# Kernel tuning notes

Hardware: AMD Instinct MI355X
Metric: run time of the kernel (lower is better)

## Reference

```python
import jax, jax.numpy as jnp
import numpy as np

EPS = 1e-5
H = 8
N_BUCKETS = 32


def _instance_norm(x, gamma, beta):
    # x: [B, N, D]; torch InstanceNorm1d normalizes over the N (length) dim
    # per channel per batch element, using biased variance.
    m = jnp.mean(x, axis=1, keepdims=True)
    v = jnp.var(x, axis=1, keepdims=True)
    return (x - m) * jax.lax.rsqrt(v + EPS) * gamma + beta


def setup_inputs() -> dict:
    key = jax.random.key(0)
    ks = jax.random.split(key, 12)
    B, N, D, d_ff = 4, 512, 128, 512
    s = 1.0 / np.sqrt(D)
    sf = 1.0 / np.sqrt(d_ff)
    u = lambda k, shape, lim: jax.random.uniform(k, shape, jnp.float32, -lim, lim)
    return {
        "h": jax.random.normal(ks[0], (B, N, D), jnp.float32),
        "coords": jax.random.uniform(ks[1], (B, N, 2), jnp.float32),
        "W_Q": u(ks[2], (D, D), s),
        "W_K": u(ks[3], (D, D), s),
        "W_V": u(ks[4], (D, D), s),
        "W_O": u(ks[5], (D, D), s),
        "emb": jax.random.normal(ks[6], (N_BUCKETS, D), jnp.float32),  # n_heads*d_k == D
        "ffn_w1": u(ks[7], (D, d_ff), s),
        "ffn_b1": u(ks[8], (d_ff,), s),
        "ffn_w2": u(ks[9], (d_ff, D), sf),
        "ffn_b2": u(ks[10], (D,), sf),
        "gamma1": jnp.ones((D,), jnp.float32),
        "beta1": jnp.zeros((D,), jnp.float32),
        "gamma2": jnp.ones((D,), jnp.float32),
        "beta2": jnp.zeros((D,), jnp.float32),
    }


def reference(h, coords, W_Q, W_K, W_V, W_O, emb, ffn_w1, ffn_b1, ffn_w2,
              ffn_b2, gamma1, beta1, gamma2, beta2):
    B, N, D = h.shape
    Dk = D // H
    Q = (h @ W_Q).reshape(B, N, H, Dk)
    K = (h @ W_K).reshape(B, N, H, Dk)
    V = (h @ W_V).reshape(B, N, H, Dk)
    # content scores: [B, H, N, N]
    scores = jnp.einsum('bnhd,bmhd->bhnm', Q, K) / np.sqrt(Dk)
    # relative-distance bucket embeddings for all (i, j) pairs
    diff = coords[:, :, None, :] - coords[:, None, :, :]          # [B,N,N,2]
    dist = jax.lax.stop_gradient(jnp.sqrt(jnp.sum(diff * diff, -1)))
    buckets = jnp.clip((dist * N_BUCKETS).astype(jnp.int32), 0, N_BUCKETS - 1)
    r = emb[buckets].reshape(B, N, N, H, Dk)                      # [B,N,N,H,Dk]
    scores = scores + jnp.einsum('bnhd,bnmhd->bhnm', Q, r)
    attn = jax.nn.softmax(scores, axis=-1)
    h_attn = jnp.einsum('bhnm,bmhd->bnhd', attn, V).reshape(B, N, D) @ W_O
    h1 = _instance_norm(h + h_attn, gamma1, beta1)
    h_ffn = jax.nn.relu(h1 @ ffn_w1 + ffn_b1) @ ffn_w2 + ffn_b2
    return _instance_norm(h1 + h_ffn, gamma2, beta2)
```

## Files before the change

### kernel.cpp

```cpp
#include <hip/hip_runtime.h>
#include <hip/hip_bf16.h>

#define B_  4
#define N_  512
#define D_  128
#define H_  8
#define DK  16
#define DFF 512
#define NB  32
#define KS  8
#define FS  8

__global__ __launch_bounds__(256) void qkv_qe_kernel(
    const float* __restrict__ A,
    const float* __restrict__ WQ, const float* __restrict__ WK, const float* __restrict__ WV,
    const float* __restrict__ emb,
    float* __restrict__ Qo, float* __restrict__ Ko, float* __restrict__ Vo,
    float* __restrict__ QE)
{
    const float* Bw = blockIdx.z == 0 ? WQ : (blockIdx.z == 1 ? WK : WV);
    float*       C  = blockIdx.z == 0 ? Qo : (blockIdx.z == 1 ? Ko : Vo);
    const int wave = threadIdx.x >> 6;
    const int lane = threadIdx.x & 63;
    const int rbase = __builtin_amdgcn_readfirstlane((blockIdx.x * 4 + wave) * 2);
    const int col = lane * 2;

    float acc[2][2] = {};
#pragma unroll 2
    for (int k0 = 0; k0 < D_; k0 += 4) {
        float4 a0 = *(const float4*)&A[(size_t)(rbase + 0) * D_ + k0];
        float4 a1 = *(const float4*)&A[(size_t)(rbase + 1) * D_ + k0];
#pragma unroll
        for (int kk = 0; kk < 4; ++kk) {
            float2 bv = *(const float2*)&Bw[(size_t)(k0 + kk) * D_ + col];
            float x0 = (&a0.x)[kk], x1 = (&a1.x)[kk];
            acc[0][0] += x0 * bv.x; acc[0][1] += x0 * bv.y;
            acc[1][0] += x1 * bv.x; acc[1][1] += x1 * bv.y;
        }
    }
    *(float2*)&C[(size_t)(rbase + 0) * D_ + col] = make_float2(acc[0][0], acc[0][1]);
    *(float2*)&C[(size_t)(rbase + 1) * D_ + col] = make_float2(acc[1][0], acc[1][1]);

    if (blockIdx.z == 0) {
        __shared__ float Qls[8][132];
        *(float2*)&Qls[wave * 2 + 0][col] = make_float2(acc[0][0], acc[0][1]);
        *(float2*)&Qls[wave * 2 + 1][col] = make_float2(acc[1][0], acc[1][1]);
        __syncthreads();
        const int r  = threadIdx.x >> 5;
        const int hh = (threadIdx.x >> 2) & 7;
        const int k0 = (threadIdx.x & 3) * 8;
        const int grow = blockIdx.x * 8 + r;
        const float4* qv = (const float4*)&Qls[r][hh * DK];
        const float4 qa = qv[0], qb = qv[1], qc = qv[2], qd = qv[3];
        float* qe_out = QE + ((size_t)grow * H_ + hh) * NB + k0;
#pragma unroll 2
        for (int k = 0; k < 8; ++k) {
            const float4* ep = (const float4*)(emb + (size_t)(k0 + k) * D_ + hh * DK);
            float4 e0 = ep[0], e1 = ep[1], e2 = ep[2], e3 = ep[3];
            float dot = qa.x*e0.x + qa.y*e0.y + qa.z*e0.z + qa.w*e0.w
                      + qb.x*e1.x + qb.y*e1.y + qb.z*e1.z + qb.w*e1.w
                      + qc.x*e2.x + qc.y*e2.y + qc.z*e2.z + qc.w*e2.w
                      + qd.x*e3.x + qd.y*e3.y + qd.z*e3.z + qd.w*e3.w;
            qe_out[k] = dot;
        }
    }
}

__global__ __launch_bounds__(256) void attn6_kernel(
    const float* __restrict__ Q, const float* __restrict__ K, const float* __restrict__ V,
    const float* __restrict__ QE, const float* __restrict__ coords,
    float* __restrict__ P)
{
    const int tid  = threadIdx.x;
    const int wave = tid >> 6;
    const int lane = tid & 63;
    const int bid  = blockIdx.x;
    const int ks    = bid & 7;
    const int chunk = (bid >> 3) & 7;
    const int h     = (bid >> 6) & (H_ - 1);
    const int b     = bid >> 9;

    const int n   = chunk * 64 + lane;
    const int row = b * N_ + n;

    __shared__ float kl[64][16];
    __shared__ float vl[64][16];
    __shared__ float qel[64][NB + 1];
    __shared__ float ckrd[64][2];
    __shared__ float accl[4][64][17];

    const size_t hdbase = (size_t)b * N_ * D_ + h * DK;

    {
        int key = tid >> 2, part = tid & 3;
        size_t g = hdbase + (size_t)(ks * 64 + key) * D_ + part * 4;
        *(float4*)&kl[key][part * 4] = *(const float4*)&K[g];
        *(float4*)&vl[key][part * 4] = *(const float4*)&V[g];
    }
    {
        int r = tid >> 2, part = tid & 3;
        const float* src = QE + ((size_t)(b * N_ + chunk * 64 + r) * H_ + h) * NB + part * 8;
#pragma unroll
        for (int j = 0; j < 8; ++j) qel[r][part * 8 + j] = src[j];
    }
    if (tid < 128)
        ((float*)ckrd)[tid] = coords[(size_t)(b * N_ + ks * 64) * 2 + tid];

    const float4* qp = (const float4*)(Q + (size_t)row * D_ + h * DK);
    const float4 q0 = qp[0], q1 = qp[1], q2 = qp[2], q3 = qp[3];
    const float cx = coords[(size_t)row * 2 + 0];
    const float cy = coords[(size_t)row * 2 + 1];

    __syncthreads();

    float l = 0.f;
    float acc[16] = {};

    const int ml0 = wave * 16;
#pragma unroll 4
    for (int i = 0; i < 16; ++i) {
        const int ml = ml0 + i;
        const float4* kp = (const float4*)&kl[ml][0];
        const float4 k0 = kp[0], k1 = kp[1], k2 = kp[2], k3 = kp[3];
        float dot = q0.x*k0.x + q0.y*k0.y + q0.z*k0.z + q0.w*k0.w
                  + q1.x*k1.x + q1.y*k1.y + q1.z*k1.z + q1.w*k1.w
                  + q2.x*k2.x + q2.y*k2.y + q2.z*k2.z + q2.w*k2.w
                  + q3.x*k3.x + q3.y*k3.y + q3.z*k3.z + q3.w*k3.w;
        float dx = cx - ckrd[ml][0], dy = cy - ckrd[ml][1];
        float dist = sqrtf(dx * dx + dy * dy);
        int bucket = (int)(dist * 32.0f);
        bucket = bucket > (NB - 1) ? (NB - 1) : bucket;
        float s = dot * 0.25f + qel[lane][bucket];
        float p = __expf(s);
        l += p;
        const float4* vp = (const float4*)&vl[ml][0];
        const float4 v0 = vp[0], v1 = vp[1], v2 = vp[2], v3 = vp[3];
        acc[0]  += p * v0.x; acc[1]  += p * v0.y; acc[2]  += p * v0.z; acc[3]  += p * v0.w;
        acc[4]  += p * v1.x; acc[5]  += p * v1.y; acc[6]  += p * v1.z; acc[7]  += p * v1.w;
        acc[8]  += p * v2.x; acc[9]  += p * v2.y; acc[10] += p * v2.z; acc[11] += p * v2.w;
        acc[12] += p * v3.x; acc[13] += p * v3.y; acc[14] += p * v3.z; acc[15] += p * v3.w;
    }

    accl[wave][lane][16] = l;
#pragma unroll
    for (int j = 0; j < 16; ++j) accl[wave][lane][j] = acc[j];
    __syncthreads();

    float* pb = P + (size_t)bid * (64 * 17);
    for (int i = tid; i < 64 * 17; i += 256) {
        int r = i / 17, j = i - r * 17;
        pb[i] = accl[0][r][j] + accl[1][r][j] + accl[2][r][j] + accl[3][r][j];
    }
}

__global__ __launch_bounds__(256) void oproj_kernel(
    const float* __restrict__ P, const float* __restrict__ WO,
    const float* __restrict__ hres, float* __restrict__ X1)
{
    const int tid = threadIdx.x;
    const int gr0 = blockIdx.x * 8;
    __shared__ float AOls[8][128];
    __shared__ float lsl[8][8];

    if (tid < 64) {
        int r = tid >> 3, hh = tid & 7;
        int gr = gr0 + r;
        int b = gr >> 9, n = gr & (N_ - 1);
        int chunk = n >> 6, rl = n & 63;
        size_t base = ((size_t)(((b * H_ + hh) * 8 + chunk) * KS)) * (64 * 17) + (size_t)rl * 17;
        float l = 0.f;
#pragma unroll
        for (int s = 0; s < KS; ++s) l += P[base + (size_t)s * (64 * 17) + 16];
        lsl[r][hh] = l;
    }

    float asum[4];
#pragma unroll
    for (int j = 0; j < 4; ++j) {
        int i = tid + j * 256;
        int r = i >> 7, d = i & 127;
        int gr = gr0 + r;
        int b = gr >> 9, n = gr & (N_ - 1);
        int chunk = n >> 6, rl = n & 63;
        int hh = d >> 4, dk = d & 15;
        size_t base = ((size_t)(((b * H_ + hh) * 8 + chunk) * KS)) * (64 * 17) + (size_t)rl * 17 + dk;
        float a = 0.f;
#pragma unroll
        for (int s = 0; s < KS; ++s) a += P[base + (size_t)s * (64 * 17)];
        asum[j] = a;
    }
    __syncthreads();
#pragma unroll
    for (int j = 0; j < 4; ++j) {
        int i = tid + j * 256;
        int r = i >> 7, d = i & 127;
        AOls[r][d] = asum[j] / lsl[r][d >> 4];
    }
    __syncthreads();

    const int wave = tid >> 6;
    const int lane = tid & 63;
    const int rl = wave * 2;
    const int grb = __builtin_amdgcn_readfirstlane(gr0 + rl);
    const int col = lane * 2;

    float acc[2][2] = {};
#pragma unroll 2
    for (int k0 = 0; k0 < D_; k0 += 4) {
        float4 a0 = *(const float4*)&AOls[rl + 0][k0];
        float4 a1 = *(const float4*)&AOls[rl + 1][k0];
#pragma unroll
        for (int kk = 0; kk < 4; ++kk) {
            float2 bv = *(const float2*)&WO[(size_t)(k0 + kk) * D_ + col];
            float x0 = (&a0.x)[kk], x1 = (&a1.x)[kk];
            acc[0][0] += x0 * bv.x; acc[0][1] += x0 * bv.y;
            acc[1][0] += x1 * bv.x; acc[1][1] += x1 * bv.y;
        }
    }
#pragma unroll
    for (int j = 0; j < 2; ++j) {
        float2 rv = *(const float2*)&hres[(size_t)(grb + j) * D_ + col];
        *(float2*)&X1[(size_t)(grb + j) * D_ + col] =
            make_float2(acc[j][0] + rv.x, acc[j][1] + rv.y);
    }
}

__global__ __launch_bounds__(256) void stats_kernel(const float* __restrict__ X,
    const float* __restrict__ gamma, const float* __restrict__ beta,
    float* __restrict__ T1, float* __restrict__ T2)
{
    const int b  = blockIdx.x >> 5;
    const int dg = blockIdx.x & 31;
    const int dl = threadIdx.x & 3;
    const int nc = threadIdx.x >> 2;
    const float* xp = X + ((size_t)b * N_ + nc * 8) * D_ + dg * 4 + dl;
    float s = 0.f, q = 0.f;
#pragma unroll
    for (int i = 0; i < 8; ++i) { float x = xp[(size_t)i * D_]; s += x; q += x * x; }
    __shared__ float rs[64][4], rq[64][4];
    rs[nc][dl] = s; rq[nc][dl] = q;
    __syncthreads();
    for (int off = 32; off >= 1; off >>= 1) {
        if (nc < off) { rs[nc][dl] += rs[nc + off][dl]; rq[nc][dl] += rq[nc + off][dl]; }
        __syncthreads();
    }
    if (threadIdx.x < 4) {
        int d = dg * 4 + threadIdx.x;
        float mean = rs[0][threadIdx.x] * (1.0f / N_);
        float var  = rq[0][threadIdx.x] * (1.0f / N_) - mean * mean;
        float r = 1.0f / sqrtf(var + 1e-5f);
        float t1 = r * gamma[d];
        T1[b * D_ + d] = t1;
        T2[b * D_ + d] = beta[d] - mean * t1;
    }
}

__global__ __launch_bounds__(256) void ffn1_kernel(
    const float* __restrict__ X1, const float* __restrict__ T1, const float* __restrict__ T2,
    const float* __restrict__ w1, const float* __restrict__ b1, float* __restrict__ F1)
{
    __shared__ float Als[16][128];
    const int gr0 = blockIdx.x * 16;
    const int b = gr0 >> 9;
#pragma unroll
    for (int i = threadIdx.x * 4; i < 16 * 128; i += 1024) {
        int r = i >> 7, c = i & 127;
        float4 x  = *(const float4*)&X1[(size_t)(gr0 + r) * D_ + c];
        float4 t1 = *(const float4*)&T1[b * D_ + c];
        float4 t2 = *(const float4*)&T2[b * D_ + c];
        float4 y;
        y.x = x.x * t1.x + t2.x; y.y = x.y * t1.y + t2.y;
        y.z = x.z * t1.z + t2.z; y.w = x.w * t1.w + t2.w;
        *(float4*)&Als[r][c] = y;
    }
    __syncthreads();

    const int wave = threadIdx.x >> 6;
    const int lane = threadIdx.x & 63;
    const int rl = wave * 4;
    const int grb = __builtin_amdgcn_readfirstlane(gr0 + rl);
    const int col = blockIdx.y * 128 + lane * 2;

    float acc[4][2] = {};
#pragma unroll 2
    for (int k0 = 0; k0 < D_; k0 += 4) {
        float4 a4[4];
#pragma unroll
        for (int j = 0; j < 4; ++j) a4[j] = *(const float4*)&Als[rl + j][k0];
#pragma unroll
        for (int kk = 0; kk < 4; ++kk) {
            float2 bv = *(const float2*)&w1[(size_t)(k0 + kk) * DFF + col];
#pragma unroll
            for (int j = 0; j < 4; ++j) {
                float a = (&a4[j].x)[kk];
                acc[j][0] += a * bv.x;
                acc[j][1] += a * bv.y;
            }
        }
    }
    float2 bb = *(const float2*)&b1[col];
#pragma unroll
    for (int j = 0; j < 4; ++j) {
        float o0 = fmaxf(acc[j][0] + bb.x, 0.f);
        float o1 = fmaxf(acc[j][1] + bb.y, 0.f);
        *(float2*)&F1[(size_t)(grb + j) * DFF + col] = make_float2(o0, o1);
    }
}

__global__ __launch_bounds__(256) void ffn2s_kernel(
    const float* __restrict__ F1, const float* __restrict__ w2, float* __restrict__ Pf)
{
    const int wave = threadIdx.x >> 6;
    const int lane = threadIdx.x & 63;
    const int rbase = __builtin_amdgcn_readfirstlane((blockIdx.x * 4 + wave) * 4);
    const int col = lane * 2;
    const int s = blockIdx.z;
    const int kbeg = s * (DFF / FS);

    float acc[4][2] = {};
#pragma unroll 2
    for (int k0 = kbeg; k0 < kbeg + DFF / FS; k0 += 4) {
        float4 a4[4];
#pragma unroll
        for (int j = 0; j < 4; ++j)
            a4[j] = *(const float4*)&F1[(size_t)(rbase + j) * DFF + k0];
#pragma unroll
        for (int kk = 0; kk < 4; ++kk) {
            float2 bv = *(const float2*)&w2[(size_t)(k0 + kk) * D_ + col];
#pragma unroll
            for (int j = 0; j < 4; ++j) {
                float a = (&a4[j].x)[kk];
                acc[j][0] += a * bv.x;
                acc[j][1] += a * bv.y;
            }
        }
    }
#pragma unroll
    for (int j = 0; j < 4; ++j)
        *(float2*)&Pf[((size_t)s * (B_ * N_) + rbase + j) * D_ + col] =
            make_float2(acc[j][0], acc[j][1]);
}

__global__ __launch_bounds__(256) void fcomb_kernel(
    const float* __restrict__ Pf, const float* __restrict__ b2,
    const float* __restrict__ X1, const float* __restrict__ T1, const float* __restrict__ T2,
    float* __restrict__ X2)
{
    int idx = (blockIdx.x * 256 + threadIdx.x) * 4;
    int d = idx & (D_ - 1);
    int b = idx >> 16;
    float4 o  = *(const float4*)&b2[d];
    float4 x1 = *(const float4*)&X1[idx];
    float4 t1 = *(const float4*)&T1[b * D_ + d];
    float4 t2 = *(const float4*)&T2[b * D_ + d];
    o.x += x1.x * t1.x + t2.x; o.y += x1.y * t1.y + t2.y;
    o.z += x1.z * t1.z + t2.z; o.w += x1.w * t1.w + t2.w;
#pragma unroll
    for (int s = 0; s < FS; ++s) {
        float4 p = *(const float4*)&Pf[(size_t)s * (B_ * N_ * D_) + idx];
        o.x += p.x; o.y += p.y; o.z += p.z; o.w += p.w;
    }
    *(float4*)&X2[idx] = o;
}

__global__ __launch_bounds__(256) void stats_apply_kernel(const float* __restrict__ X,
    const float* __restrict__ gamma, const float* __restrict__ beta,
    float* __restrict__ Y)
{
    const int b  = blockIdx.x >> 5;
    const int dg = blockIdx.x & 31;
    const int dl = threadIdx.x & 3;
    const int nc = threadIdx.x >> 2;
    const float* xp = X + ((size_t)b * N_ + nc * 8) * D_ + dg * 4 + dl;
    float s = 0.f, q = 0.f;
#pragma unroll
    for (int i = 0; i < 8; ++i) { float x = xp[(size_t)i * D_]; s += x; q += x * x; }
    __shared__ float rs[64][4], rq[64][4];
    __shared__ float t1l[4], t2l[4];
    rs[nc][dl] = s; rq[nc][dl] = q;
    __syncthreads();
    for (int off = 32; off >= 1; off >>= 1) {
        if (nc < off) { rs[nc][dl] += rs[nc + off][dl]; rq[nc][dl] += rq[nc + off][dl]; }
        __syncthreads();
    }
    if (threadIdx.x < 4) {
        int d = dg * 4 + threadIdx.x;
        float mean = rs[0][threadIdx.x] * (1.0f / N_);
        float var  = rq[0][threadIdx.x] * (1.0f / N_) - mean * mean;
        float r = 1.0f / sqrtf(var + 1e-5f);
        float t1 = r * gamma[d];
        t1l[threadIdx.x] = t1;
        t2l[threadIdx.x] = beta[d] - mean * t1;
    }
    __syncthreads();
    const float t1 = t1l[dl], t2 = t2l[dl];
    float* yp = Y + ((size_t)b * N_ + nc * 8) * D_ + dg * 4 + dl;
#pragma unroll
    for (int i = 0; i < 8; ++i) yp[(size_t)i * D_] = xp[(size_t)i * D_] * t1 + t2;
}

extern "C" void kernel_launch(void* const* d_in, const int* in_sizes, int n_in,
                              void* d_out, int out_size, void* d_ws, size_t ws_size,
                              hipStream_t stream)
{
    const float* h      = (const float*)d_in[0];
    const float* coords = (const float*)d_in[1];
    const float* W_Q    = (const float*)d_in[2];
    const float* W_K    = (const float*)d_in[3];
    const float* W_V    = (const float*)d_in[4];
    const float* W_O    = (const float*)d_in[5];
    const float* emb    = (const float*)d_in[6];
    const float* w1     = (const float*)d_in[7];
    const float* b1     = (const float*)d_in[8];
    const float* w2     = (const float*)d_in[9];
    const float* b2     = (const float*)d_in[10];
    const float* g1     = (const float*)d_in[11];
    const float* be1    = (const float*)d_in[12];
    const float* g2     = (const float*)d_in[13];
    const float* be2    = (const float*)d_in[14];
    float* out = (float*)d_out;

    float* ws = (float*)d_ws;
    const size_t R = (size_t)B_ * N_;
    float* Qb  = ws;
    float* Kb  = Qb + R * D_;
    float* Vb  = Kb + R * D_;
    float* QEb = Vb + R * D_;
    float* X1  = QEb + R * H_ * NB;
    float* F1  = X1 + R * D_;
    float* X2  = F1 + R * DFF;
    float* Pb  = X2 + R * D_;
    float* Pf  = Pb + (size_t)2048 * 64 * 17;
    float* T1a = Pf + (size_t)FS * R * D_;
    float* T2a = T1a + B_ * D_;

    qkv_qe_kernel<<<dim3(256, 1, 3), 256, 0, stream>>>(
        h, W_Q, W_K, W_V, emb, Qb, Kb, Vb, QEb);
    attn6_kernel<<<dim3(2048), 256, 0, stream>>>(Qb, Kb, Vb, QEb, coords, Pb);
    oproj_kernel<<<dim3((int)R / 8), 256, 0, stream>>>(Pb, W_O, h, X1);
    stats_kernel<<<dim3(B_ * 32), 256, 0, stream>>>(X1, g1, be1, T1a, T2a);
    ffn1_kernel<<<dim3(128, 4), 256, 0, stream>>>(X1, T1a, T2a, w1, b1, F1);
    ffn2s_kernel<<<dim3(128, 1, FS), 256, 0, stream>>>(F1, w2, Pf);
    fcomb_kernel<<<dim3((int)(R * D_) / 1024), 256, 0, stream>>>(Pf, b2, X1, T1a, T2a, X2);
    stats_apply_kernel<<<dim3(B_ * 32), 256, 0, stream>>>(X2, g2, be2, out);
}
```

Before: 84.56 us.

## Halve attention key splits, loop two key tiles per block, retile oproj

Result: no change. 86.20 us (+1.9%).

```diff
diff --git a/kernel.cpp b/kernel.cpp
--- a/kernel.cpp
+++ b/kernel.cpp
@@ -8,8 +8,8 @@
 #define DK  16
 #define DFF 512
 #define NB  32
-#define KS  8
-#define FS  8
+#define KS  4
+#define FS  4
 
 __global__ __launch_bounds__(256) void qkv_qe_kernel(
     const float* __restrict__ A,
@@ -57,16 +57,16 @@
         for (int k = 0; k < 8; ++k) {
             const float4* ep = (const float4*)(emb + (size_t)(k0 + k) * D_ + hh * DK);
             float4 e0 = ep[0], e1 = ep[1], e2 = ep[2], e3 = ep[3];
-            float dot = qa.x*e0.x + qa.y*e0.y + qa.z*e0.z + qa.w*e0.w
-                      + qb.x*e1.x + qb.y*e1.y + qb.z*e1.z + qb.w*e1.w
-                      + qc.x*e2.x + qc.y*e2.y + qc.z*e2.z + qc.w*e2.w
-                      + qd.x*e3.x + qd.y*e3.y + qd.z*e3.z + qd.w*e3.w;
-            qe_out[k] = dot;
-        }
-    }
-}
-
-__global__ __launch_bounds__(256) void attn6_kernel(
+            float d0 = fmaf(qa.x,e0.x, fmaf(qa.y,e0.y, fmaf(qa.z,e0.z, qa.w*e0.w)));
+            float d1 = fmaf(qb.x,e1.x, fmaf(qb.y,e1.y, fmaf(qb.z,e1.z, qb.w*e1.w)));
+            float d2 = fmaf(qc.x,e2.x, fmaf(qc.y,e2.y, fmaf(qc.z,e2.z, qc.w*e2.w)));
+            float d3 = fmaf(qd.x,e3.x, fmaf(qd.y,e3.y, fmaf(qd.z,e3.z, qd.w*e3.w)));
+            qe_out[k] = (d0 + d1) + (d2 + d3);
+        }
+    }
+}
+
+__global__ __launch_bounds__(256) void attn7_kernel(
     const float* __restrict__ Q, const float* __restrict__ K, const float* __restrict__ V,
     const float* __restrict__ QE, const float* __restrict__ coords,
     float* __restrict__ P)
@@ -75,72 +75,74 @@
     const int wave = tid >> 6;
     const int lane = tid & 63;
     const int bid  = blockIdx.x;
-    const int ks    = bid & 7;
-    const int chunk = (bid >> 3) & 7;
-    const int h     = (bid >> 6) & (H_ - 1);
-    const int b     = bid >> 9;
-
-    const int n   = chunk * 64 + lane;
-    const int row = b * N_ + n;
+    const int ks    = bid & 3;
+    const int chunk = (bid >> 2) & 7;
+    const int h     = (bid >> 5) & (H_ - 1);
+    const int b     = bid >> 8;
+    const int row = b * N_ + chunk * 64 + lane;
 
     __shared__ float kl[64][16];
     __shared__ float vl[64][16];
     __shared__ float qel[64][NB + 1];
-    __shared__ float ckrd[64][2];
+    __shared__ float ckrd[128][2];
     __shared__ float accl[4][64][17];
 
     const size_t hdbase = (size_t)b * N_ * D_ + h * DK;
 
-    {
-        int key = tid >> 2, part = tid & 3;
-        size_t g = hdbase + (size_t)(ks * 64 + key) * D_ + part * 4;
-        *(float4*)&kl[key][part * 4] = *(const float4*)&K[g];
-        *(float4*)&vl[key][part * 4] = *(const float4*)&V[g];
-    }
     {
         int r = tid >> 2, part = tid & 3;
         const float* src = QE + ((size_t)(b * N_ + chunk * 64 + r) * H_ + h) * NB + part * 8;
 #pragma unroll
         for (int j = 0; j < 8; ++j) qel[r][part * 8 + j] = src[j];
     }
-    if (tid < 128)
-        ((float*)ckrd)[tid] = coords[(size_t)(b * N_ + ks * 64) * 2 + tid];
+    ((float*)ckrd)[tid] = coords[(size_t)(b * N_ + ks * 128) * 2 + tid];
 
     const float4* qp = (const float4*)(Q + (size_t)row * D_ + h * DK);
     const float4 q0 = qp[0], q1 = qp[1], q2 = qp[2], q3 = qp[3];
     const float cx = coords[(size_t)row * 2 + 0];
     const float cy = coords[(size_t)row * 2 + 1];
 
-    __syncthreads();
-
     float l = 0.f;
     float acc[16] = {};
 
-    const int ml0 = wave * 16;
+    for (int rnd = 0; rnd < 2; ++rnd) {
+        if (rnd) __syncthreads();
+        {
+            int key = tid >> 2, part = tid & 3;
+            size_t g = hdbase + (size_t)(ks * 128 + rnd * 64 + key) * D_ + part * 4;
+            *(float4*)&kl[key][part * 4] = *(const float4*)&K[g];
+            *(float4*)&vl[key][part * 4] = *(const float4*)&V[g];
+        }
+        __syncthreads();
+
+        const int ml0 = wave * 16;
 #pragma unroll 4
-    for (int i = 0; i < 16; ++i) {
-        const int ml = ml0 + i;
-        const float4* kp = (const float4*)&kl[ml][0];
-        const float4 k0 = kp[0], k1 = kp[1], k2 = kp[2], k3 = kp[3];
-        float dot = q0.x*k0.x + q0.y*k0.y + q0.z*k0.z + q0.w*k0.w
-                  + q1.x*k1.x + q1.y*k1.y + q1.z*k1.z + q1.w*k1.w
-                  + q2.x*k2.x + q2.y*k2.y + q2.z*k2.z + q2.w*k2.w
-                  + q3.x*k3.x + q3.y*k3.y + q3.z*k3.z + q3.w*k3.w;
-        float dx = cx - ckrd[ml][0], dy = cy - ckrd[ml][1];
-        float dist = sqrtf(dx * dx + dy * dy);
-        int bucket = (int)(dist * 32.0f);
-        bucket = bucket > (NB - 1) ? (NB - 1) : bucket;
-        float s = dot * 0.25f + qel[lane][bucket];
-        float p = __expf(s);
-        l += p;
-        const float4* vp = (const float4*)&vl[ml][0];
-        const float4 v0 = vp[0], v1 = vp[1], v2 = vp[2], v3 = vp[3];
-        acc[0]  += p * v0.x; acc[1]  += p * v0.y; acc[2]  += p * v0.z; acc[3]  += p * v0.w;
-        acc[4]  += p * v1.x; acc[5]  += p * v1.y; acc[6]  += p * v1.z; acc[7]  += p * v1.w;
-        acc[8]  += p * v2.x; acc[9]  += p * v2.y; acc[10] += p * v2.z; acc[11] += p * v2.w;
-        acc[12] += p * v3.x; acc[13] += p * v3.y; acc[14] += p * v3.z; acc[15] += p * v3.w;
-    }
-
+        for (int i = 0; i < 16; ++i) {
+            const int ml = ml0 + i;
+            const int mc = rnd * 64 + ml;
+            float dx = cx - ckrd[mc][0], dy = cy - ckrd[mc][1];
+            float dist = sqrtf(fmaf(dx, dx, dy * dy));
+            int bucket = (int)(dist * 32.0f);
+            bucket = bucket > (NB - 1) ? (NB - 1) : bucket;
+            float qe = qel[lane][bucket];
+            const float4* kp = (const float4*)&kl[ml][0];
+            const float4 k0 = kp[0], k1 = kp[1], k2 = kp[2], k3 = kp[3];
+            float d0 = fmaf(q0.x,k0.x, fmaf(q0.y,k0.y, fmaf(q0.z,k0.z, q0.w*k0.w)));
+            float d1 = fmaf(q1.x,k1.x, fmaf(q1.y,k1.y, fmaf(q1.z,k1.z, q1.w*k1.w)));
+            float d2 = fmaf(q2.x,k2.x, fmaf(q2.y,k2.y, fmaf(q2.z,k2.z, q2.w*k2.w)));
+            float d3 = fmaf(q3.x,k3.x, fmaf(q3.y,k3.y, fmaf(q3.z,k3.z, q3.w*k3.w)));
+            float p = __expf(fmaf((d0 + d1) + (d2 + d3), 0.25f, qe));
+            l += p;
+            const float4* vp = (const float4*)&vl[ml][0];
+            const float4 v0 = vp[0], v1 = vp[1], v2 = vp[2], v3 = vp[3];
+            acc[0]  += p * v0.x; acc[1]  += p * v0.y; acc[2]  += p * v0.z; acc[3]  += p * v0.w;
+            acc[4]  += p * v1.x; acc[5]  += p * v1.y; acc[6]  += p * v1.z; acc[7]  += p * v1.w;
+            acc[8]  += p * v2.x; acc[9]  += p * v2.y; acc[10] += p * v2.z; acc[11] += p * v2.w;
+            acc[12] += p * v3.x; acc[13] += p * v3.y; acc[14] += p * v3.z; acc[15] += p * v3.w;
+        }
+    }
+
+    __syncthreads();
     accl[wave][lane][16] = l;
 #pragma unroll
     for (int j = 0; j < 16; ++j) accl[wave][lane][j] = acc[j];
@@ -158,11 +160,11 @@
     const float* __restrict__ hres, float* __restrict__ X1)
 {
     const int tid = threadIdx.x;
-    const int gr0 = blockIdx.x * 8;
-    __shared__ float AOls[8][128];
-    __shared__ float lsl[8][8];
-
-    if (tid < 64) {
+    const int gr0 = blockIdx.x * 4;
+    __shared__ float AOls[4][128];
+    __shared__ float lsl[4][8];
+
+    if (tid < 32) {
         int r = tid >> 3, hh = tid & 7;
         int gr = gr0 + r;
         int b = gr >> 9, n = gr & (N_ - 1);
@@ -173,10 +175,9 @@
         for (int s = 0; s < KS; ++s) l += P[base + (size_t)s * (64 * 17) + 16];
         lsl[r][hh] = l;
     }
-
-    float asum[4];
-#pragma unroll
-    for (int j = 0; j < 4; ++j) {
+    float asum[2];
+#pragma unroll
+    for (int j = 0; j < 2; ++j) {
         int i = tid + j * 256;
         int r = i >> 7, d = i & 127;
         int gr = gr0 + r;
@@ -184,14 +185,14 @@
         int chunk = n >> 6, rl = n & 63;
         int hh = d >> 4, dk = d & 15;
         size_t base = ((size_t)(((b * H_ + hh) * 8 + chunk) * KS)) * (64 * 17) + (size_t)rl * 17 + dk;
-        float a = 0.f;
-#pragma unroll
-        for (int s = 0; s < KS; ++s) a += P[base + (size_t)s * (64 * 17)];
-        asum[j] = a;
-    }
-    __syncthreads();
-#pragma unroll
-    for (int j = 0; j < 4; ++j) {
+        float s = 0.f;
+#pragma unroll
+        for (int ss = 0; ss < KS; ++ss) s += P[base + (size_t)ss * (64 * 17)];
+        asum[j] = s;
+    }
+    __syncthreads();
+#pragma unroll
+    for (int j = 0; j < 2; ++j) {
         int i = tid + j * 256;
         int r = i >> 7, d = i & 127;
         AOls[r][d] = asum[j] / lsl[r][d >> 4];
@@ -200,29 +201,21 @@
 
     const int wave = tid >> 6;
     const int lane = tid & 63;
-    const int rl = wave * 2;
-    const int grb = __builtin_amdgcn_readfirstlane(gr0 + rl);
     const int col = lane * 2;
-
-    float acc[2][2] = {};
+    float acc0 = 0.f, acc1 = 0.f;
 #pragma unroll 2
     for (int k0 = 0; k0 < D_; k0 += 4) {
-        float4 a0 = *(const float4*)&AOls[rl + 0][k0];
-        float4 a1 = *(const float4*)&AOls[rl + 1][k0];
+        float4 av = *(const float4*)&AOls[wave][k0];
 #pragma unroll
         for (int kk = 0; kk < 4; ++kk) {
             float2 bv = *(const float2*)&WO[(size_t)(k0 + kk) * D_ + col];
-            float x0 = (&a0.x)[kk], x1 = (&a1.x)[kk];
-            acc[0][0] += x0 * bv.x; acc[0][1] += x0 * bv.y;
-            acc[1][0] += x1 * bv.x; acc[1][1] += x1 * bv.y;
-        }
-    }
-#pragma unroll
-    for (int j = 0; j < 2; ++j) {
-        float2 rv = *(const float2*)&hres[(size_t)(grb + j) * D_ + col];
-        *(float2*)&X1[(size_t)(grb + j) * D_ + col] =
-            make_float2(acc[j][0] + rv.x, acc[j][1] + rv.y);
-    }
+            float x = (&av.x)[kk];
+            acc0 += x * bv.x; acc1 += x * bv.y;
+        }
+    }
+    const int gr = gr0 + wave;
+    float2 rv = *(const float2*)&hres[(size_t)gr * D_ + col];
+    *(float2*)&X1[(size_t)gr * D_ + col] = make_float2(acc0 + rv.x, acc1 + rv.y);
 }
 
 __global__ __launch_bounds__(256) void stats_kernel(const float* __restrict__ X,
@@ -278,7 +271,6 @@
     const int wave = threadIdx.x >> 6;
     const int lane = threadIdx.x & 63;
     const int rl = wave * 4;
-    const int grb = __builtin_amdgcn_readfirstlane(gr0 + rl);
     const int col = blockIdx.y * 128 + lane * 2;
 
     float acc[4][2] = {};
@@ -292,9 +284,8 @@
             float2 bv = *(const float2*)&w1[(size_t)(k0 + kk) * DFF + col];
 #pragma unroll
             for (int j = 0; j < 4; ++j) {
-                float a = (&a4[j].x)[kk];
-                acc[j][0] += a * bv.x;
-                acc[j][1] += a * bv.y;
+                float x = (&a4[j].x)[kk];
+                acc[j][0] += x * bv.x; acc[j][1] += x * bv.y;
             }
         }
     }
@@ -303,7 +294,7 @@
     for (int j = 0; j < 4; ++j) {
         float o0 = fmaxf(acc[j][0] + bb.x, 0.f);
         float o1 = fmaxf(acc[j][1] + bb.y, 0.f);
-        *(float2*)&F1[(size_t)(grb + j) * DFF + col] = make_float2(o0, o1);
+        *(float2*)&F1[(size_t)(gr0 + rl + j) * DFF + col] = make_float2(o0, o1);
     }
 }
 
@@ -329,9 +320,8 @@
             float2 bv = *(const float2*)&w2[(size_t)(k0 + kk) * D_ + col];
 #pragma unroll
             for (int j = 0; j < 4; ++j) {
-                float a = (&a4[j].x)[kk];
-                acc[j][0] += a * bv.x;
-                acc[j][1] += a * bv.y;
+                float x = (&a4[j].x)[kk];
+                acc[j][0] += x * bv.x; acc[j][1] += x * bv.y;
             }
         }
     }
@@ -430,14 +420,14 @@
     float* F1  = X1 + R * D_;
     float* X2  = F1 + R * DFF;
     float* Pb  = X2 + R * D_;
-    float* Pf  = Pb + (size_t)2048 * 64 * 17;
+    float* Pf  = Pb + (size_t)1024 * 64 * 17;
     float* T1a = Pf + (size_t)FS * R * D_;
     float* T2a = T1a + B_ * D_;
 
     qkv_qe_kernel<<<dim3(256, 1, 3), 256, 0, stream>>>(
         h, W_Q, W_K, W_V, emb, Qb, Kb, Vb, QEb);
-    attn6_kernel<<<dim3(2048), 256, 0, stream>>>(Qb, Kb, Vb, QEb, coords, Pb);
-    oproj_kernel<<<dim3((int)R / 8), 256, 0, stream>>>(Pb, W_O, h, X1);
+    attn7_kernel<<<dim3(1024), 256, 0, stream>>>(Qb, Kb, Vb, QEb, coords, Pb);
+    oproj_kernel<<<dim3((int)R / 4), 256, 0, stream>>>(Pb, W_O, h, X1);
     stats_kernel<<<dim3(B_ * 32), 256, 0, stream>>>(X1, g1, be1, T1a, T2a);
     ffn1_kernel<<<dim3(128, 4), 256, 0, stream>>>(X1, T1a, T2a, w1, b1, F1);
     ffn2s_kernel<<<dim3(128, 1, FS), 256, 0, stream>>>(F1, w2, Pf);
```

## Fuse FFN2 split-K reduction and residual combine into one kernel via LDS

Applied to the files above, without the earlier changes.

New measurement: 80.73 us. 1.05x faster.

```diff
diff --git a/kernel.cpp b/kernel.cpp
--- a/kernel.cpp
+++ b/kernel.cpp
@@ -9,7 +9,6 @@
 #define DFF 512
 #define NB  32
 #define KS  8
-#define FS  8
 
 __global__ __launch_bounds__(256) void qkv_qe_kernel(
     const float* __restrict__ A,
@@ -57,11 +56,11 @@
         for (int k = 0; k < 8; ++k) {
             const float4* ep = (const float4*)(emb + (size_t)(k0 + k) * D_ + hh * DK);
             float4 e0 = ep[0], e1 = ep[1], e2 = ep[2], e3 = ep[3];
-            float dot = qa.x*e0.x + qa.y*e0.y + qa.z*e0.z + qa.w*e0.w
-                      + qb.x*e1.x + qb.y*e1.y + qb.z*e1.z + qb.w*e1.w
-                      + qc.x*e2.x + qc.y*e2.y + qc.z*e2.z + qc.w*e2.w
-                      + qd.x*e3.x + qd.y*e3.y + qd.z*e3.z + qd.w*e3.w;
-            qe_out[k] = dot;
+            float d0 = fmaf(qa.x,e0.x, fmaf(qa.y,e0.y, fmaf(qa.z,e0.z, qa.w*e0.w)));
+            float d1 = fmaf(qb.x,e1.x, fmaf(qb.y,e1.y, fmaf(qb.z,e1.z, qb.w*e1.w)));
+            float d2 = fmaf(qc.x,e2.x, fmaf(qc.y,e2.y, fmaf(qc.z,e2.z, qc.w*e2.w)));
+            float d3 = fmaf(qd.x,e3.x, fmaf(qd.y,e3.y, fmaf(qd.z,e3.z, qd.w*e3.w)));
+            qe_out[k] = (d0 + d1) + (d2 + d3);
         }
     }
 }
@@ -79,9 +78,7 @@
     const int chunk = (bid >> 3) & 7;
     const int h     = (bid >> 6) & (H_ - 1);
     const int b     = bid >> 9;
-
-    const int n   = chunk * 64 + lane;
-    const int row = b * N_ + n;
+    const int row = b * N_ + chunk * 64 + lane;
 
     __shared__ float kl[64][16];
     __shared__ float vl[64][16];
@@ -90,7 +87,6 @@
     __shared__ float accl[4][64][17];
 
     const size_t hdbase = (size_t)b * N_ * D_ + h * DK;
-
     {
         int key = tid >> 2, part = tid & 3;
         size_t g = hdbase + (size_t)(ks * 64 + key) * D_ + part * 4;
@@ -115,23 +111,22 @@
 
     float l = 0.f;
     float acc[16] = {};
-
     const int ml0 = wave * 16;
 #pragma unroll 4
     for (int i = 0; i < 16; ++i) {
         const int ml = ml0 + i;
+        float dx = cx - ckrd[ml][0], dy = cy - ckrd[ml][1];
+        float dist = sqrtf(fmaf(dx, dx, dy * dy));
+        int bucket = (int)(dist * 32.0f);
+        bucket = bucket > (NB - 1) ? (NB - 1) : bucket;
+        float qe = qel[lane][bucket];
         const float4* kp = (const float4*)&kl[ml][0];
         const float4 k0 = kp[0], k1 = kp[1], k2 = kp[2], k3 = kp[3];
-        float dot = q0.x*k0.x + q0.y*k0.y + q0.z*k0.z + q0.w*k0.w
-                  + q1.x*k1.x + q1.y*k1.y + q1.z*k1.z + q1.w*k1.w
-                  + q2.x*k2.x + q2.y*k2.y + q2.z*k2.z + q2.w*k2.w
-                  + q3.x*k3.x + q3.y*k3.y + q3.z*k3.z + q3.w*k3.w;
-        float dx = cx - ckrd[ml][0], dy = cy - ckrd[ml][1];
-        float dist = sqrtf(dx * dx + dy * dy);
-        int bucket = (int)(dist * 32.0f);
-        bucket = bucket > (NB - 1) ? (NB - 1) : bucket;
-        float s = dot * 0.25f + qel[lane][bucket];
-        float p = __expf(s);
+        float d0 = fmaf(q0.x,k0.x, fmaf(q0.y,k0.y, fmaf(q0.z,k0.z, q0.w*k0.w)));
+        float d1 = fmaf(q1.x,k1.x, fmaf(q1.y,k1.y, fmaf(q1.z,k1.z, q1.w*k1.w)));
+        float d2 = fmaf(q2.x,k2.x, fmaf(q2.y,k2.y, fmaf(q2.z,k2.z, q2.w*k2.w)));
+        float d3 = fmaf(q3.x,k3.x, fmaf(q3.y,k3.y, fmaf(q3.z,k3.z, q3.w*k3.w)));
+        float p = __expf(fmaf((d0 + d1) + (d2 + d3), 0.25f, qe));
         l += p;
         const float4* vp = (const float4*)&vl[ml][0];
         const float4 v0 = vp[0], v1 = vp[1], v2 = vp[2], v3 = vp[3];
@@ -173,7 +168,6 @@
         for (int s = 0; s < KS; ++s) l += P[base + (size_t)s * (64 * 17) + 16];
         lsl[r][hh] = l;
     }
-
     float asum[4];
 #pragma unroll
     for (int j = 0; j < 4; ++j) {
@@ -184,10 +178,10 @@
         int chunk = n >> 6, rl = n & 63;
         int hh = d >> 4, dk = d & 15;
         size_t base = ((size_t)(((b * H_ + hh) * 8 + chunk) * KS)) * (64 * 17) + (size_t)rl * 17 + dk;
-        float a = 0.f;
-#pragma unroll
-        for (int s = 0; s < KS; ++s) a += P[base + (size_t)s * (64 * 17)];
-        asum[j] = a;
+        float s = 0.f;
+#pragma unroll
+        for (int ss = 0; ss < KS; ++ss) s += P[base + (size_t)ss * (64 * 17)];
+        asum[j] = s;
     }
     __syncthreads();
 #pragma unroll
@@ -278,7 +272,6 @@
     const int wave = threadIdx.x >> 6;
     const int lane = threadIdx.x & 63;
     const int rl = wave * 4;
-    const int grb = __builtin_amdgcn_readfirstlane(gr0 + rl);
     const int col = blockIdx.y * 128 + lane * 2;
 
     float acc[4][2] = {};
@@ -292,9 +285,8 @@
             float2 bv = *(const float2*)&w1[(size_t)(k0 + kk) * DFF + col];
 #pragma unroll
             for (int j = 0; j < 4; ++j) {
-                float a = (&a4[j].x)[kk];
-                acc[j][0] += a * bv.x;
-                acc[j][1] += a * bv.y;
+                float x = (&a4[j].x)[kk];
+                acc[j][0] += x * bv.x; acc[j][1] += x * bv.y;
             }
         }
     }
@@ -303,64 +295,57 @@
     for (int j = 0; j < 4; ++j) {
         float o0 = fmaxf(acc[j][0] + bb.x, 0.f);
         float o1 = fmaxf(acc[j][1] + bb.y, 0.f);
-        *(float2*)&F1[(size_t)(grb + j) * DFF + col] = make_float2(o0, o1);
-    }
-}
-
-__global__ __launch_bounds__(256) void ffn2s_kernel(
-    const float* __restrict__ F1, const float* __restrict__ w2, float* __restrict__ Pf)
-{
-    const int wave = threadIdx.x >> 6;
-    const int lane = threadIdx.x & 63;
-    const int rbase = __builtin_amdgcn_readfirstlane((blockIdx.x * 4 + wave) * 4);
+        *(float2*)&F1[(size_t)(gr0 + rl + j) * DFF + col] = make_float2(o0, o1);
+    }
+}
+
+__global__ __launch_bounds__(256) void ffn2f_kernel(
+    const float* __restrict__ F1, const float* __restrict__ w2, const float* __restrict__ b2,
+    const float* __restrict__ X1, const float* __restrict__ T1, const float* __restrict__ T2,
+    float* __restrict__ X2)
+{
+    const int tid = threadIdx.x;
+    const int wave = tid >> 6;
+    const int lane = tid & 63;
+    const int gr0 = __builtin_amdgcn_readfirstlane(blockIdx.x * 4);
+    const int kbeg = __builtin_amdgcn_readfirstlane(wave * 128);
     const int col = lane * 2;
-    const int s = blockIdx.z;
-    const int kbeg = s * (DFF / FS);
+
+    __shared__ float part[4][4][128];
 
     float acc[4][2] = {};
 #pragma unroll 2
-    for (int k0 = kbeg; k0 < kbeg + DFF / FS; k0 += 4) {
+    for (int k0 = kbeg; k0 < kbeg + 128; k0 += 4) {
         float4 a4[4];
 #pragma unroll
         for (int j = 0; j < 4; ++j)
-            a4[j] = *(const float4*)&F1[(size_t)(rbase + j) * DFF + k0];
+            a4[j] = *(const float4*)&F1[(size_t)(gr0 + j) * DFF + k0];
 #pragma unroll
         for (int kk = 0; kk < 4; ++kk) {
             float2 bv = *(const float2*)&w2[(size_t)(k0 + kk) * D_ + col];
 #pragma unroll
             for (int j = 0; j < 4; ++j) {
-                float a = (&a4[j].x)[kk];
-                acc[j][0] += a * bv.x;
-                acc[j][1] += a * bv.y;
+                float x = (&a4[j].x)[kk];
+                acc[j][0] += x * bv.x; acc[j][1] += x * bv.y;
             }
         }
     }
 #pragma unroll
     for (int j = 0; j < 4; ++j)
-        *(float2*)&Pf[((size_t)s * (B_ * N_) + rbase + j) * D_ + col] =
-            make_float2(acc[j][0], acc[j][1]);
-}
-
-__global__ __launch_bounds__(256) void fcomb_kernel(
-    const float* __restrict__ Pf, const float* __restrict__ b2,
-    const float* __restrict__ X1, const float* __restrict__ T1, const float* __restrict__ T2,
-    float* __restrict__ X2)
-{
-    int idx = (blockIdx.x * 256 + threadIdx.x) * 4;
-    int d = idx & (D_ - 1);
-    int b = idx >> 16;
-    float4 o  = *(const float4*)&b2[d];
-    float4 x1 = *(const float4*)&X1[idx];
-    float4 t1 = *(const float4*)&T1[b * D_ + d];
-    float4 t2 = *(const float4*)&T2[b * D_ + d];
-    o.x += x1.x * t1.x + t2.x; o.y += x1.y * t1.y + t2.y;
-    o.z += x1.z * t1.z + t2.z; o.w += x1.w * t1.w + t2.w;
-#pragma unroll
-    for (int s = 0; s < FS; ++s) {
-        float4 p = *(const float4*)&Pf[(size_t)s * (B_ * N_ * D_) + idx];
-        o.x += p.x; o.y += p.y; o.z += p.z; o.w += p.w;
-    }
-    *(float4*)&X2[idx] = o;
+        *(float2*)&part[wave][j][col] = make_float2(acc[j][0], acc[j][1]);
+    __syncthreads();
+
+#pragma unroll
+    for (int e = 0; e < 2; ++e) {
+        int i = tid + e * 256;
+        int r = i >> 7, c = i & 127;
+        int row = gr0 + r;
+        int b = row >> 9;
+        float s = part[0][r][c] + part[1][r][c] + part[2][r][c] + part[3][r][c];
+        float x1 = X1[(size_t)row * D_ + c];
+        float o = s + b2[c] + (x1 * T1[b * D_ + c] + T2[b * D_ + c]);
+        X2[(size_t)row * D_ + c] = o;
+    }
 }
 
 __global__ __launch_bounds__(256) void stats_apply_kernel(const float* __restrict__ X,
@@ -430,8 +415,7 @@
     float* F1  = X1 + R * D_;
     float* X2  = F1 + R * DFF;
     float* Pb  = X2 + R * D_;
-    float* Pf  = Pb + (size_t)2048 * 64 * 17;
-    float* T1a = Pf + (size_t)FS * R * D_;
+    float* T1a = Pb + (size_t)2048 * 64 * 17;
     float* T2a = T1a + B_ * D_;
 
     qkv_qe_kernel<<<dim3(256, 1, 3), 256, 0, stream>>>(
@@ -440,7 +424,6 @@
     oproj_kernel<<<dim3((int)R / 8), 256, 0, stream>>>(Pb, W_O, h, X1);
     stats_kernel<<<dim3(B_ * 32), 256, 0, stream>>>(X1, g1, be1, T1a, T2a);
     ffn1_kernel<<<dim3(128, 4), 256, 0, stream>>>(X1, T1a, T2a, w1, b1, F1);
-    ffn2s_kernel<<<dim3(128, 1, FS), 256, 0, stream>>>(F1, w2, Pf);
-    fcomb_kernel<<<dim3((int)(R * D_) / 1024), 256, 0, stream>>>(Pf, b2, X1, T1a, T2a, X2);
+    ffn2f_kernel<<<dim3((int)R / 4), 256, 0, stream>>>(F1, w2, b2, X1, T1a, T2a, X2);
     stats_apply_kernel<<<dim3(B_ * 32), 256, 0, stream>>>(X2, g2, be2, out);
 }
```
